# Kernel optimization log

Hardware: AMD Instinct MI355X
Metric: run time of the kernel (lower is better)

Reference implementation:

```python
import jax, jax.numpy as jnp
import numpy as np

N = 50000      # nodes
E = 800000     # edges (avg degree 16)
D = 96         # input_size == output_size
C = 10         # n_class
STEPS = 4      # num_layers -> GGNN propagation steps


def setup_inputs() -> dict:
    key = jax.random.key(0)
    ks = jax.random.split(key, 12)
    s = 1.0 / np.sqrt(D)
    return {
        "x": jax.random.normal(ks[0], (N, D), dtype=jnp.float32),
        "src": jax.random.randint(ks[1], (E,), 0, N, dtype=jnp.int32),
        "dst": jax.random.randint(ks[2], (E,), 0, N, dtype=jnp.int32),
        # edge message transform (DGL GatedGraphConv: Linear(out, out) per etype, 1 etype)
        "W_e": jax.random.normal(ks[3], (D, D), dtype=jnp.float32) * s,
        "b_e": jax.random.normal(ks[4], (D,), dtype=jnp.float32) * s,
        # GRUCell params (torch layout: rows ordered r, z, n)
        "W_ih": jax.random.normal(ks[5], (3 * D, D), dtype=jnp.float32) * s,
        "W_hh": jax.random.normal(ks[6], (3 * D, D), dtype=jnp.float32) * s,
        "b_ih": jax.random.normal(ks[7], (3 * D,), dtype=jnp.float32) * s,
        "b_hh": jax.random.normal(ks[8], (3 * D,), dtype=jnp.float32) * s,
        # classifier head
        "W_fc": jax.random.normal(ks[9], (C, D), dtype=jnp.float32) * s,
        "b_fc": jax.random.normal(ks[10], (C,), dtype=jnp.float32) * s,
    }


def _gru_cell(a, h, W_ih, W_hh, b_ih, b_hh):
    # torch.nn.GRUCell math; gate order r, z, n
    gx = a @ W_ih.T + b_ih            # [N, 3D]
    gh = h @ W_hh.T + b_hh            # [N, 3D]
    xr, xz, xn = jnp.split(gx, 3, axis=-1)
    hr, hz, hn = jnp.split(gh, 3, axis=-1)
    r = jax.nn.sigmoid(xr + hr)
    z = jax.nn.sigmoid(xz + hz)
    n = jnp.tanh(xn + r * hn)
    return (1.0 - z) * n + z * h


def reference(x, src, dst, W_e, b_e, W_ih, W_hh, b_ih, b_hh, W_fc, b_fc):
    h = x  # in_feats == out_feats, no padding needed
    for _ in range(STEPS):
        m = h @ W_e.T + b_e                                  # per-node transform [N, D]
        a = jax.ops.segment_sum(m[src], dst, num_segments=N) # gather + scatter-add [N, D]
        h = _gru_cell(a, h, W_ih, W_hh, b_ih, b_hh)
    logits = jax.nn.elu(h) @ W_fc.T + b_fc                   # [N, C]
    return logits
```

## Files before the change

### kernel.cpp

```cpp
#include <hip/hip_runtime.h>

static constexpr int D = 96;
static constexpr int G3 = 3 * D;
static constexpr int NSTEPS = 4;
static constexpr int NT = 18;
static constexpr int SCAN_BLK = 1024;
static constexpr int SLP = 104;
static constexpr int PLS = 97;
static constexpr int PLANE = 16 * PLS;

typedef __attribute__((ext_vector_type(8))) _Float16 f16x8;
typedef __attribute__((ext_vector_type(4))) _Float16 f16x4;
typedef __attribute__((ext_vector_type(4))) float f32x4;

__device__ __forceinline__ f16x8 load_a_frag(const _Float16* __restrict__ base,
                                             int r0, int lane, int kc) {
  int row = r0 + (lane & 15);
  int k0 = kc * 32 + ((lane >> 4) << 3);
  return *(const f16x8*)(base + (size_t)row * D + k0);
}

__device__ __forceinline__ f16x8 load_b_swz(const _Float16* __restrict__ W,
                                            int t, int kc, int lane) {
  return *(const f16x8*)(W + (((size_t)t * 3 + kc) * 64 + lane) * 8);
}


__global__ void convert_x_kernel(const float* __restrict__ x,
                                 _Float16* __restrict__ h, int total4) {
  int i = blockIdx.x * blockDim.x + threadIdx.x;
  if (i >= total4) return;
  float4 v = ((const float4*)x)[i];
  f16x4 o;
  o[0] = (_Float16)v.x; o[1] = (_Float16)v.y;
  o[2] = (_Float16)v.z; o[3] = (_Float16)v.w;
  *(f16x4*)(h + (size_t)i * 4) = o;
}

__global__ void compute_wx_kernel(const float* __restrict__ Wih,
                                  const float* __restrict__ We,
                                  const float* __restrict__ be,
                                  float* __restrict__ Wx,
                                  float* __restrict__ bxe) {
  int idx = blockIdx.x * blockDim.x + threadIdx.x;
  if (idx < G3 * D) {
    int r = idx / D, k = idx - r * D;
    float acc = 0.f;
    for (int c = 0; c < D; ++c) acc += Wih[r * D + c] * We[c * D + k];
    Wx[idx] = acc;
  } else if (idx < G3 * D + G3) {
    int r = idx - G3 * D;
    float acc = 0.f;
    for (int c = 0; c < D; ++c) acc += Wih[r * D + c] * be[c];
    bxe[r] = acc;
  }
}

__global__ void swizzle_f16_kernel(const float* __restrict__ Wx,
                                   const float* __restrict__ Whh,
                                   _Float16* __restrict__ WxF,
                                   _Float16* __restrict__ WhhF) {
  int idx = blockIdx.x * blockDim.x + threadIdx.x;
  if (idx >= 2 * NT * 3 * 64) return;
  int mat = idx / (NT * 3 * 64);
  int rem = idx - mat * (NT * 3 * 64);
  int t = rem / (3 * 64);
  int rem2 = rem - t * (3 * 64);
  int kc = rem2 >> 6;
  int lane = rem2 & 63;
  int c = t * 16 + (lane & 15);
  int k0 = kc * 32 + ((lane >> 4) << 3);
  const float* W = mat ? Whh : Wx;
  _Float16* dF = mat ? WhhF : WxF;
  f16x8 o;
#pragma unroll
  for (int j = 0; j < 8; ++j) o[j] = (_Float16)W[(size_t)c * D + k0 + j];
  *(f16x8*)(dF + (((size_t)t * 3 + kc) * 64 + lane) * 8) = o;
}


__global__ void hist_kernel(const int* __restrict__ dst, int* __restrict__ counts, int E) {
  int e = blockIdx.x * blockDim.x + threadIdx.x;
  if (e < E) atomicAdd(&counts[dst[e]], 1);
}

__global__ void partial_sum_kernel(const int* __restrict__ counts,
                                   int* __restrict__ blk_sums, int n) {
  __shared__ int red[256];
  int base = blockIdx.x * SCAN_BLK;
  int tid = threadIdx.x;
  int s = 0;
#pragma unroll
  for (int j = 0; j < 4; ++j) {
    int i = base + j * 256 + tid;
    if (i < n) s += counts[i];
  }
  red[tid] = s;
  __syncthreads();
  for (int off = 128; off > 0; off >>= 1) {
    if (tid < off) red[tid] += red[tid + off];
    __syncthreads();
  }
  if (tid == 0) blk_sums[blockIdx.x] = red[0];
}

__global__ void scan_offsets_kernel(const int* __restrict__ blk_sums,
                                    int* __restrict__ blk_off,
                                    int* __restrict__ row_ptr, int nb, int n) {
  __shared__ int lds[64];
  int tid = threadIdx.x;
  if (tid < nb) lds[tid] = blk_sums[tid];
  __syncthreads();
  if (tid == 0) {
    int run = 0;
    for (int i = 0; i < nb; ++i) { blk_off[i] = run; run += lds[i]; }
    row_ptr[n] = run;
  }
}

__global__ void block_scan_kernel(const int* __restrict__ counts,
                                  const int* __restrict__ blk_off,
                                  int* __restrict__ row_ptr, int n) {
  __shared__ int red[256];
  int base = blockIdx.x * SCAN_BLK;
  int tid = threadIdx.x;
  int i0 = base + tid * 4;
  int v0 = 0, v1 = 0, v2 = 0, v3 = 0;
  if (i0 + 3 < n) {
    int4 c = *(const int4*)(counts + i0);
    v0 = c.x; v1 = c.y; v2 = c.z; v3 = c.w;
  } else {
    if (i0 < n) v0 = counts[i0];
    if (i0 + 1 < n) v1 = counts[i0 + 1];
    if (i0 + 2 < n) v2 = counts[i0 + 2];
  }
  int tsum = v0 + v1 + v2 + v3;
  red[tid] = tsum;
  __syncthreads();
  for (int off = 1; off < 256; off <<= 1) {
    int t = (tid >= off) ? red[tid - off] : 0;
    __syncthreads();
    red[tid] += t;
    __syncthreads();
  }
  int excl = blk_off[blockIdx.x] + red[tid] - tsum;
  if (i0 < n) row_ptr[i0] = excl;
  if (i0 + 1 < n) row_ptr[i0 + 1] = excl + v0;
  if (i0 + 2 < n) row_ptr[i0 + 2] = excl + v0 + v1;
  if (i0 + 3 < n) row_ptr[i0 + 3] = excl + v0 + v1 + v2;
}

__global__ void fill_kernel(const int* __restrict__ src, const int* __restrict__ dst,
                            const int* __restrict__ row_ptr,
                            int* __restrict__ fillc, int* __restrict__ csr_src, int E) {
  int e = blockIdx.x * blockDim.x + threadIdx.x;
  if (e >= E) return;
  int t = dst[e];
  int pos = row_ptr[t] + atomicAdd(&fillc[t], 1);
  csr_src[pos] = src[e];
}


__device__ __forceinline__ void gru_epilogue(const float* lds,
                                             const _Float16* __restrict__ h,
                                             _Float16* __restrict__ hout,
                                             const int* __restrict__ row_ptr,
                                             const float* __restrict__ bxe,
                                             const float* __restrict__ bih,
                                             const float* __restrict__ bhh,
                                             int base_row, int tid) {
#pragma unroll
  for (int j = 0; j < 4; ++j) {
    int e = tid + j * 384;
    int row = e / D;
    int col = e - row * D;
    int grow = base_row + row;
    int a = row * PLS + col;
    float degf = (float)(row_ptr[grow + 1] - row_ptr[grow]);
    float R  = lds[a] + lds[PLANE + a];
    float Z  = lds[2 * PLANE + a] + lds[3 * PLANE + a];
    float XN = lds[4 * PLANE + a];
    float HN = lds[5 * PLANE + a];
    float rg = 1.0f / (1.0f + __expf(-(R + bih[col] + bhh[col] + degf * bxe[col])));
    float zg = 1.0f / (1.0f + __expf(-(Z + bih[D + col] + bhh[D + col] + degf * bxe[D + col])));
    float ng = tanhf(XN + bih[2 * D + col] + degf * bxe[2 * D + col] + rg * (HN + bhh[2 * D + col]));
    float hv = (float)h[(size_t)grow * D + col];
    hout[(size_t)grow * D + col] = (_Float16)((1.0f - zg) * ng + zg * hv);
  }
}

__global__ __launch_bounds__(384) void gru_fused_kernel(
    const _Float16* __restrict__ h, _Float16* __restrict__ hout,
    const int* __restrict__ row_ptr, const int* __restrict__ csr_src,
    const _Float16* __restrict__ WxF, const _Float16* __restrict__ WhhF,
    const float* __restrict__ bxe, const float* __restrict__ bih,
    const float* __restrict__ bhh, int n) {
  __shared__ float lds[6 * PLANE];
  __shared__ _Float16 sl[32][SLP];
  int r0 = blockIdx.x << 5;
  int tid = threadIdx.x;
  int w = tid >> 6;
  int lane = tid & 63;

  {
    int row = tid / 12;
    int part = tid - row * 12;
    int grow = r0 + row;
    float acc[8];
#pragma unroll
    for (int j = 0; j < 8; ++j) acc[j] = 0.f;
    if (grow < n) {
      int beg = row_ptr[grow], end = row_ptr[grow + 1];
      int e = beg;
      for (; e + 3 < end; e += 4) {
        int s0 = csr_src[e], s1 = csr_src[e + 1], s2 = csr_src[e + 2], s3 = csr_src[e + 3];
        f16x8 v0 = *(const f16x8*)(h + (size_t)s0 * D + part * 8);
        f16x8 v1 = *(const f16x8*)(h + (size_t)s1 * D + part * 8);
        f16x8 v2 = *(const f16x8*)(h + (size_t)s2 * D + part * 8);
        f16x8 v3 = *(const f16x8*)(h + (size_t)s3 * D + part * 8);
#pragma unroll
        for (int j = 0; j < 8; ++j)
          acc[j] += ((float)v0[j] + (float)v1[j]) + ((float)v2[j] + (float)v3[j]);
      }
      for (; e < end; ++e) {
        f16x8 v = *(const f16x8*)(h + (size_t)csr_src[e] * D + part * 8);
#pragma unroll
        for (int j = 0; j < 8; ++j) acc[j] += (float)v[j];
      }
    }
    f16x8 o;
#pragma unroll
    for (int j = 0; j < 8; ++j) o[j] = (_Float16)acc[j];
    *(f16x8*)&sl[row][part * 8] = o;
  }
  __syncthreads();

  const int opS = (w < 3) ? 1 : 0;
  const _Float16* WF = opS ? WxF : WhhF;
  const int wg = opS ? w : (w - 3);
  const int t0 = wg * 6;
  const int plane = wg * 2 + (opS ? 0 : 1);

  f16x8 a0[3], a1[3];
  if (opS) {
#pragma unroll
    for (int kc = 0; kc < 3; ++kc) {
      int k0 = kc * 32 + ((lane >> 4) << 3);
      a0[kc] = *(const f16x8*)&sl[lane & 15][k0];
      a1[kc] = *(const f16x8*)&sl[16 + (lane & 15)][k0];
    }
  } else {
#pragma unroll
    for (int kc = 0; kc < 3; ++kc) {
      a0[kc] = load_a_frag(h, r0, lane, kc);
      a1[kc] = load_a_frag(h, r0 + 16, lane, kc);
    }
  }

  f32x4 acc0[6], acc1[6];
#pragma unroll
  for (int t = 0; t < 6; ++t) {
    acc0[t] = (f32x4){0.f, 0.f, 0.f, 0.f};
    acc1[t] = (f32x4){0.f, 0.f, 0.f, 0.f};
  }

#pragma unroll
  for (int ct = 0; ct < 6; ++ct)
#pragma unroll
    for (int kc = 0; kc < 3; ++kc) {
      f16x8 b = load_b_swz(WF, t0 + ct, kc, lane);
      acc0[ct] = __builtin_amdgcn_mfma_f32_16x16x32_f16(a0[kc], b, acc0[ct], 0, 0, 0);
      acc1[ct] = __builtin_amdgcn_mfma_f32_16x16x32_f16(a1[kc], b, acc1[ct], 0, 0, 0);
    }

  int col_l = lane & 15;
  int rq = (lane >> 4) << 2;
#pragma unroll
  for (int ct = 0; ct < 6; ++ct)
#pragma unroll
    for (int q = 0; q < 4; ++q)
      lds[plane * PLANE + (rq + q) * PLS + ct * 16 + col_l] = acc0[ct][q];
  __syncthreads();
  gru_epilogue(lds, h, hout, row_ptr, bxe, bih, bhh, r0, tid);
  __syncthreads();
  if (r0 + 16 < n) {
#pragma unroll
    for (int ct = 0; ct < 6; ++ct)
#pragma unroll
      for (int q = 0; q < 4; ++q)
        lds[plane * PLANE + (rq + q) * PLS + ct * 16 + col_l] = acc1[ct][q];
    __syncthreads();
    gru_epilogue(lds, h, hout, row_ptr, bxe, bih, bhh, r0 + 16, tid);
  }
}

__global__ void head_kernel(const _Float16* __restrict__ h,
                            const float* __restrict__ Wfc,
                            const float* __restrict__ bfc,
                            float* __restrict__ out,
                            int n, int C) {
  int idx = blockIdx.x * blockDim.x + threadIdx.x;
  if (idx >= n * C) return;
  int i = idx / C;
  int c = idx - i * C;
  const _Float16* hr = h + (size_t)i * D;
  const float* wr = Wfc + (size_t)c * D;
  float acc = bfc[c];
#pragma unroll 8
  for (int k = 0; k < D; ++k) {
    float hv = (float)hr[k];
    float e = hv > 0.0f ? hv : (__expf(hv) - 1.0f);
    acc += e * wr[k];
  }
  out[idx] = acc;
}

extern "C" void kernel_launch(void* const* d_in, const int* in_sizes, int n_in,
                              void* d_out, int out_size, void* d_ws, size_t ws_size,
                              hipStream_t stream) {
  const float* x    = (const float*)d_in[0];
  const int*   src  = (const int*)d_in[1];
  const int*   dst  = (const int*)d_in[2];
  const float* W_e  = (const float*)d_in[3];
  const float* b_e  = (const float*)d_in[4];
  const float* W_ih = (const float*)d_in[5];
  const float* W_hh = (const float*)d_in[6];
  const float* b_ih = (const float*)d_in[7];
  const float* b_hh = (const float*)d_in[8];
  const float* W_fc = (const float*)d_in[9];
  const float* b_fc = (const float*)d_in[10];

  const int n = in_sizes[0] / D;
  const int E = in_sizes[1];
  const int C = out_size / n;

  _Float16* hA = (_Float16*)d_ws;
  _Float16* hB = hA + (size_t)n * D;
  float* Wx    = (float*)(hB + (size_t)n * D);
  _Float16* WxF  = (_Float16*)(Wx + (size_t)G3 * D);
  _Float16* WhhF = WxF + (size_t)G3 * D;
  float* bxe   = (float*)(WhhF + (size_t)G3 * D);
  int* counts  = (int*)(bxe + G3);
  int* fillc   = counts + n;
  int* row_ptr = fillc + n;
  int* csr_src = row_ptr + (n + 1);
  int* blk_sums = csr_src + E;
  int* blk_off  = blk_sums + 64;

  const int threads = 256;
  const int nb = (n + SCAN_BLK - 1) / SCAN_BLK;

  (void)hipMemsetAsync(counts, 0, (size_t)2 * n * sizeof(int), stream);
  hist_kernel<<<(E + threads - 1) / threads, threads, 0, stream>>>(dst, counts, E);
  partial_sum_kernel<<<nb, 256, 0, stream>>>(counts, blk_sums, n);
  scan_offsets_kernel<<<1, 64, 0, stream>>>(blk_sums, blk_off, row_ptr, nb, n);
  block_scan_kernel<<<nb, 256, 0, stream>>>(counts, blk_off, row_ptr, n);
  fill_kernel<<<(E + threads - 1) / threads, threads, 0, stream>>>(src, dst, row_ptr,
                                                                   fillc, csr_src, E);
  compute_wx_kernel<<<(G3 * D + G3 + threads - 1) / threads, threads, 0, stream>>>(
      W_ih, W_e, b_e, Wx, bxe);
  swizzle_f16_kernel<<<(2 * NT * 3 * 64 + threads - 1) / threads, threads, 0, stream>>>(
      Wx, W_hh, WxF, WhhF);
  convert_x_kernel<<<((n * D / 4) + threads - 1) / threads, threads, 0, stream>>>(
      x, hA, n * D / 4);

  const int gridG = (n + 31) / 32;

  const _Float16* hcur = hA;
  _Float16* hnext = hB;
  for (int step = 0; step < NSTEPS; ++step) {
    gru_fused_kernel<<<gridG, 384, 0, stream>>>(hcur, hnext, row_ptr, csr_src,
                                                WxF, WhhF, bxe, b_ih, b_hh, n);
    const _Float16* t = hcur; hcur = hnext; hnext = (_Float16*)t;
  }

  const int gridH = (n * C + threads - 1) / threads;
  head_kernel<<<gridH, threads, 0, stream>>>(hcur, W_fc, b_fc, (float*)d_out, n, C);
}
```

Baseline: 356.3 us.

## Use 16-bit CSR source indices, deepen gather unroll, alias aggregation tile into LDS

CSR source indices are now stored as unsigned short, halving index traffic in the fill and gather stages; this only works while the node count stays below 65536. The neighbor gather loop is unrolled to 8 edges with a 4-edge tail, so more independent row loads are in flight per thread. The aggregated-feature tile now shares storage with the GRU accumulation planes instead of using its own array, which cuts LDS use per block and may raise occupancy. In exchange it adds a second barrier after the A-fragment loads.

```diff
diff --git a/kernel.cpp b/kernel.cpp
--- a/kernel.cpp
+++ b/kernel.cpp
@@ -152,12 +152,13 @@
 
 __global__ void fill_kernel(const int* __restrict__ src, const int* __restrict__ dst,
                             const int* __restrict__ row_ptr,
-                            int* __restrict__ fillc, int* __restrict__ csr_src, int E) {
+                            int* __restrict__ fillc,
+                            unsigned short* __restrict__ csr_src, int E) {
   int e = blockIdx.x * blockDim.x + threadIdx.x;
   if (e >= E) return;
   int t = dst[e];
   int pos = row_ptr[t] + atomicAdd(&fillc[t], 1);
-  csr_src[pos] = src[e];
+  csr_src[pos] = (unsigned short)src[e];
 }
 
 
@@ -191,12 +192,12 @@
 
 __global__ __launch_bounds__(384) void gru_fused_kernel(
     const _Float16* __restrict__ h, _Float16* __restrict__ hout,
-    const int* __restrict__ row_ptr, const int* __restrict__ csr_src,
+    const int* __restrict__ row_ptr, const unsigned short* __restrict__ csr_src,
     const _Float16* __restrict__ WxF, const _Float16* __restrict__ WhhF,
     const float* __restrict__ bxe, const float* __restrict__ bih,
     const float* __restrict__ bhh, int n) {
   __shared__ float lds[6 * PLANE];
-  __shared__ _Float16 sl[32][SLP];
+  _Float16* sl = (_Float16*)&lds[4 * PLANE];
   int r0 = blockIdx.x << 5;
   int tid = threadIdx.x;
   int w = tid >> 6;
@@ -211,19 +212,34 @@
     for (int j = 0; j < 8; ++j) acc[j] = 0.f;
     if (grow < n) {
       int beg = row_ptr[grow], end = row_ptr[grow + 1];
+      const _Float16* hp = h + (size_t)part * 8;
       int e = beg;
-      for (; e + 3 < end; e += 4) {
-        int s0 = csr_src[e], s1 = csr_src[e + 1], s2 = csr_src[e + 2], s3 = csr_src[e + 3];
-        f16x8 v0 = *(const f16x8*)(h + (size_t)s0 * D + part * 8);
-        f16x8 v1 = *(const f16x8*)(h + (size_t)s1 * D + part * 8);
-        f16x8 v2 = *(const f16x8*)(h + (size_t)s2 * D + part * 8);
-        f16x8 v3 = *(const f16x8*)(h + (size_t)s3 * D + part * 8);
+      for (; e + 7 < end; e += 8) {
+        f16x8 v0 = *(const f16x8*)(hp + (size_t)csr_src[e] * D);
+        f16x8 v1 = *(const f16x8*)(hp + (size_t)csr_src[e + 1] * D);
+        f16x8 v2 = *(const f16x8*)(hp + (size_t)csr_src[e + 2] * D);
+        f16x8 v3 = *(const f16x8*)(hp + (size_t)csr_src[e + 3] * D);
+        f16x8 v4 = *(const f16x8*)(hp + (size_t)csr_src[e + 4] * D);
+        f16x8 v5 = *(const f16x8*)(hp + (size_t)csr_src[e + 5] * D);
+        f16x8 v6 = *(const f16x8*)(hp + (size_t)csr_src[e + 6] * D);
+        f16x8 v7 = *(const f16x8*)(hp + (size_t)csr_src[e + 7] * D);
+#pragma unroll
+        for (int j = 0; j < 8; ++j)
+          acc[j] += (((float)v0[j] + (float)v1[j]) + ((float)v2[j] + (float)v3[j])) +
+                    (((float)v4[j] + (float)v5[j]) + ((float)v6[j] + (float)v7[j]));
+      }
+      if (e + 3 < end) {
+        f16x8 v0 = *(const f16x8*)(hp + (size_t)csr_src[e] * D);
+        f16x8 v1 = *(const f16x8*)(hp + (size_t)csr_src[e + 1] * D);
+        f16x8 v2 = *(const f16x8*)(hp + (size_t)csr_src[e + 2] * D);
+        f16x8 v3 = *(const f16x8*)(hp + (size_t)csr_src[e + 3] * D);
 #pragma unroll
         for (int j = 0; j < 8; ++j)
           acc[j] += ((float)v0[j] + (float)v1[j]) + ((float)v2[j] + (float)v3[j]);
+        e += 4;
       }
       for (; e < end; ++e) {
-        f16x8 v = *(const f16x8*)(h + (size_t)csr_src[e] * D + part * 8);
+        f16x8 v = *(const f16x8*)(hp + (size_t)csr_src[e] * D);
 #pragma unroll
         for (int j = 0; j < 8; ++j) acc[j] += (float)v[j];
       }
@@ -231,7 +247,7 @@
     f16x8 o;
 #pragma unroll
     for (int j = 0; j < 8; ++j) o[j] = (_Float16)acc[j];
-    *(f16x8*)&sl[row][part * 8] = o;
+    *(f16x8*)&sl[row * SLP + part * 8] = o;
   }
   __syncthreads();
 
@@ -246,8 +262,8 @@
 #pragma unroll
     for (int kc = 0; kc < 3; ++kc) {
       int k0 = kc * 32 + ((lane >> 4) << 3);
-      a0[kc] = *(const f16x8*)&sl[lane & 15][k0];
-      a1[kc] = *(const f16x8*)&sl[16 + (lane & 15)][k0];
+      a0[kc] = *(const f16x8*)&sl[(lane & 15) * SLP + k0];
+      a1[kc] = *(const f16x8*)&sl[(16 + (lane & 15)) * SLP + k0];
     }
   } else {
 #pragma unroll
@@ -256,6 +272,7 @@
       a1[kc] = load_a_frag(h, r0 + 16, lane, kc);
     }
   }
+  __syncthreads();
 
   f32x4 acc0[6], acc1[6];
 #pragma unroll
@@ -343,8 +360,8 @@
   int* counts  = (int*)(bxe + G3);
   int* fillc   = counts + n;
   int* row_ptr = fillc + n;
-  int* csr_src = row_ptr + (n + 1);
-  int* blk_sums = csr_src + E;
+  unsigned short* csr_src = (unsigned short*)(row_ptr + (n + 1));
+  int* blk_sums = (int*)(csr_src + E);
   int* blk_off  = blk_sums + 64;
 
   const int threads = 256;
```

Measured after the change: 348.1 us. -2.3%, faster.
